# Kernel tuning notes

Hardware: AMD Instinct MI355X
Metric: run time of the kernel (lower is better)

## Reference

```python
import jax, jax.numpy as jnp
import numpy as np

EMBED_DIM = 1024
NUM_HEADS = 16
HEAD_DIM = EMBED_DIM // NUM_HEADS


def setup_inputs() -> dict:
    key = jax.random.key(0)
    ks = jax.random.split(key, 10)
    s = 1.0 / np.sqrt(EMBED_DIM)
    x = jax.random.normal(ks[0], (2, 2048, EMBED_DIM), dtype=jnp.float32)
    Wq = jax.random.uniform(ks[1], (EMBED_DIM, EMBED_DIM), jnp.float32, -s, s)
    bq = jax.random.uniform(ks[2], (EMBED_DIM,), jnp.float32, -s, s)
    Wk = jax.random.uniform(ks[3], (EMBED_DIM, EMBED_DIM), jnp.float32, -s, s)
    bk = jax.random.uniform(ks[4], (EMBED_DIM,), jnp.float32, -s, s)
    Wv = jax.random.uniform(ks[5], (EMBED_DIM, EMBED_DIM), jnp.float32, -s, s)
    bv = jax.random.uniform(ks[6], (EMBED_DIM,), jnp.float32, -s, s)
    Wo = jax.random.uniform(ks[7], (EMBED_DIM, EMBED_DIM), jnp.float32, -s, s)
    bo = jax.random.uniform(ks[8], (EMBED_DIM,), jnp.float32, -s, s)
    return {"x": x, "Wq": Wq, "bq": bq, "Wk": Wk, "bk": bk,
            "Wv": Wv, "bv": bv, "Wo": Wo, "bo": bo}


def reference(x, Wq, bq, Wk, bk, Wv, bv, Wo, bo):
    b, s, e = x.shape
    h, d = NUM_HEADS, HEAD_DIM
    scale = d ** -0.5
    # projections (torch Linear: x @ W.T + b; here W stored as [in, out])
    q = (x @ Wq + bq).reshape(b, s, h, d)
    k = (x @ Wk + bk).reshape(b, s, h, d)
    v = (x @ Wv + bv).reshape(b, s, h, d)
    logits = jnp.einsum('bqhd,bkhd->bhqk', q, k) * scale
    causal = jnp.tril(jnp.ones((s, s), dtype=bool))  # keep lower triangle
    logits = jnp.where(causal, logits, -jnp.inf)
    attn = jax.nn.softmax(logits, axis=-1)
    out = jnp.einsum('bhqk,bkhd->bqhd', attn, v).reshape(b, s, e)
    return out @ Wo + bo
```

## Files before the change

### kernel.cpp

```cpp
#include <hip/hip_runtime.h>


#define EMB 1024
#define SEQ 2048
#define NB 2
#define NH 16
#define HD 64

#define QSCALE 0.18033688011112042f

typedef float f32x4 __attribute__((ext_vector_type(4)));
typedef float f32x16 __attribute__((ext_vector_type(16)));
typedef float floatx4 __attribute__((ext_vector_type(4)));
typedef short short8 __attribute__((ext_vector_type(8)));
typedef __bf16 bf16x8 __attribute__((ext_vector_type(8)));
typedef __bf16 bf16x2 __attribute__((ext_vector_type(2)));
typedef unsigned short ushortx4 __attribute__((ext_vector_type(4)));
typedef unsigned int uintx4 __attribute__((ext_vector_type(4)));
typedef int int2v __attribute__((ext_vector_type(2)));

__device__ __forceinline__ unsigned short bf16u(float f) {
  __bf16 h = (__bf16)f;
  return __builtin_bit_cast(unsigned short, h);
}

__device__ __forceinline__ unsigned pkbf(float lo, float hi) {
  bf16x2 v;
  v[0] = (__bf16)lo;
  v[1] = (__bf16)hi;
  return __builtin_bit_cast(unsigned, v);
}

__device__ __forceinline__ f32x4 mfma16(short8 a, short8 b, f32x4 c) {
  return __builtin_amdgcn_mfma_f32_16x16x32_bf16(
      __builtin_bit_cast(bf16x8, a), __builtin_bit_cast(bf16x8, b), c, 0, 0, 0);
}

__device__ __forceinline__ f32x16 mfma32(short8 a, short8 b, f32x16 c) {
  return __builtin_amdgcn_mfma_f32_32x32x16_bf16(
      __builtin_bit_cast(bf16x8, a), __builtin_bit_cast(bf16x8, b), c, 0, 0, 0);
}

__device__ __forceinline__ void plswap(unsigned& a, unsigned& b) {
  int2v r = __builtin_amdgcn_permlane32_swap((int)a, (int)b, false, false);
  a = (unsigned)r[0];
  b = (unsigned)r[1];
}

__device__ __forceinline__ void gload16(const void* g, void* lds) {
  __builtin_amdgcn_global_load_lds(
      (const __attribute__((address_space(1))) unsigned int*)g,
      (__attribute__((address_space(3))) unsigned int*)lds, 16, 0, 0);
}

__global__ __launch_bounds__(256) void cvt_x_kernel(
    const float* __restrict__ x, unsigned short* __restrict__ out) {
  const int idx = (blockIdx.x * 256 + threadIdx.x) * 4;
  floatx4 v = *(const floatx4*)(x + idx);
  ushortx4 o;
  #pragma unroll
  for (int i = 0; i < 4; ++i) o[i] = bf16u(v[i]);
  *(ushortx4*)(out + idx) = o;
}

__global__ __launch_bounds__(256) void cvt_w4_kernel(
    const float* __restrict__ W0, const float* __restrict__ W1,
    const float* __restrict__ W2, const float* __restrict__ W3,
    unsigned short* __restrict__ T0, unsigned short* __restrict__ T1,
    unsigned short* __restrict__ T2, unsigned short* __restrict__ T3) {
  __shared__ unsigned short tile[32][33];
  const int z = blockIdx.z;
  const float* W = (z == 0) ? W0 : (z == 1) ? W1 : (z == 2) ? W2 : W3;
  unsigned short* WT = (z == 0) ? T0 : (z == 1) ? T1 : (z == 2) ? T2 : T3;
  const int k0 = blockIdx.x * 32, n0 = blockIdx.y * 32;
  const int t = threadIdx.x;
  const int r = t >> 3, c = (t & 7) * 4;
  floatx4 v = *(const floatx4*)(W + (k0 + r) * EMB + n0 + c);
  #pragma unroll
  for (int i = 0; i < 4; ++i) tile[r][c + i] = bf16u(v[i]);
  __syncthreads();
  ushortx4 o;
  #pragma unroll
  for (int i = 0; i < 4; ++i) o[i] = tile[c + i][r];
  *(ushortx4*)(WT + (n0 + r) * EMB + k0 + c) = o;
}

#define GEMM_KLOOP(OP1, OP2)                                                 \
    for (int kk = 0; kk < 64; kk += 32) {                                    \
      short8 a[4], b[4];                                                     \
      _Pragma("unroll")                                                      \
      for (int i = 0; i < 4; ++i)                                            \
        a[i] = *(const short8*)(As + (wr * 64 + i * 16 + ln) * 64 + kk + g * 8); \
      _Pragma("unroll")                                                      \
      for (int j = 0; j < 4; ++j)                                            \
        b[j] = *(const short8*)(Bs + (wc * 64 + j * 16 + ln) * 64 + kk + g * 8); \
      _Pragma("unroll")                                                      \
      for (int i = 0; i < 4; ++i)                                            \
        _Pragma("unroll")                                                    \
        for (int j = 0; j < 4; ++j)                                          \
          acc[i][j] = mfma16(OP1, OP2, acc[i][j]);                           \
    }

#define GEMM_STAGE(Aptr, Bptr, kt_, buf_)                                    \
    do {                                                                     \
      const int kb_ = (kt_) * 64;                                            \
      _Pragma("unroll")                                                      \
      for (int it = 0; it < 4; ++it) {                                       \
        const int chunk = w * 4 + it;                                        \
        const int lin = chunk * 64 + l;                                      \
        const int row = lin >> 3, col = (lin & 7) * 8;                       \
        gload16(Aptr + (m0 + row) * EMB + kb_ + col,                         \
                (char*)&AsB[buf_][0] + chunk * 1024);                        \
        gload16(Bptr + (n0 + row) * EMB + kb_ + col,                         \
                (char*)&BsB[buf_][0] + chunk * 1024);                        \
      }                                                                      \
    } while (0)

__global__ __launch_bounds__(256) void gemm_qkv_kernel(
    const unsigned short* __restrict__ Xb,
    const unsigned short* __restrict__ W0, const unsigned short* __restrict__ W1,
    const unsigned short* __restrict__ W2,
    const float* __restrict__ b0, const float* __restrict__ b1,
    const float* __restrict__ b2,
    unsigned short* __restrict__ Qo, unsigned short* __restrict__ Ko,
    unsigned short* __restrict__ Vo) {
  __shared__ __align__(16) unsigned short AsB[2][128 * 64];
  __shared__ __align__(16) unsigned short BsB[2][128 * 64];
  const int z = blockIdx.z;
  const unsigned short* Wt = (z == 0) ? W0 : ((z == 1) ? W1 : W2);
  const float* bias = (z == 0) ? b0 : ((z == 1) ? b1 : b2);
  const bool sw = (z != 2);
  const int m0 = blockIdx.y * 128, n0 = blockIdx.x * 128;
  const int tid = threadIdx.x, l = tid & 63, w = tid >> 6;
  const int g = l >> 4, ln = l & 15;
  const int wr = w >> 1, wc = w & 1;

  f32x4 acc[4][4];
  #pragma unroll
  for (int i = 0; i < 4; ++i)
    #pragma unroll
    for (int j = 0; j < 4; ++j) acc[i][j] = (f32x4){0.f, 0.f, 0.f, 0.f};

  GEMM_STAGE(Xb, Wt, 0, 0);
  #pragma unroll 1
  for (int kt = 0; kt < 16; ++kt) {
    const int cur = kt & 1;
    if (kt + 1 < 16) {
      GEMM_STAGE(Xb, Wt, kt + 1, cur ^ 1);
      asm volatile("s_waitcnt vmcnt(8)" ::: "memory");
    } else {
      asm volatile("s_waitcnt vmcnt(0)" ::: "memory");
    }
    __builtin_amdgcn_s_barrier();
    const unsigned short* As = &AsB[cur][0];
    const unsigned short* Bs = &BsB[cur][0];
    if (sw) {
      GEMM_KLOOP(b[j], a[i])
    } else {
      GEMM_KLOOP(a[i], b[j])
    }
    asm volatile("" ::: "memory");
    __builtin_amdgcn_s_barrier();
  }

  const int mb = m0 + wr * 64, nb = n0 + wc * 64;
  if (sw) {
    unsigned short* dst = (z == 0) ? Qo : Ko;
    const float osc = (z == 0) ? QSCALE : 1.0f;
    #pragma unroll
    for (int j = 0; j < 4; ++j) {
      const int n = nb + j * 16 + 4 * g;
      floatx4 bv_ = *(const floatx4*)(bias + n);
      const int h = n >> 6, d = n & 63;
      #pragma unroll
      for (int i = 0; i < 4; ++i) {
        const int m = mb + i * 16 + ln;
        const int bb = m >> 11, ss = m & 2047;
        ushortx4 o;
        #pragma unroll
        for (int e = 0; e < 4; ++e) o[e] = bf16u((acc[i][j][e] + bv_[e]) * osc);
        *(ushortx4*)(dst + ((bb * NH + h) * SEQ + ss) * HD + d) = o;
      }
    }
  } else {
    #pragma unroll
    for (int j = 0; j < 4; ++j) {
      const int n = nb + j * 16 + ln;
      const float bgain = bias[n];
      const int h = n >> 6, d = n & 63;
      #pragma unroll
      for (int i = 0; i < 4; ++i) {
        const int mf = mb + i * 16 + 4 * g;
        const int bb = mf >> 11, ss = mf & 2047;
        ushortx4 o;
        #pragma unroll
        for (int e = 0; e < 4; ++e) o[e] = bf16u(acc[i][j][e] + bgain);
        *(ushortx4*)(Vo + ((bb * NH + h) * HD + d) * SEQ + ss) = o;
      }
    }
  }
}

__global__ __launch_bounds__(256) void attn_kernel(
    const unsigned short* __restrict__ Q, const unsigned short* __restrict__ K,
    const unsigned short* __restrict__ Vt, unsigned short* __restrict__ O) {
  __shared__ __align__(16) unsigned short Kt[2][128 * 64];
  __shared__ __align__(16) unsigned short Vl[2][64 * 128];
  const int id = blockIdx.x;
  const int bh = id & 31;
  const int grp = id >> 5;
  const int T = (grp < 8) ? (15 - grp) : (grp - 8);
  const int h = bh & 15, b = bh >> 4;
  const int tid = threadIdx.x, l = tid & 63, w = tid >> 6;
  const int q32 = l & 31;
  const int hi = l >> 5;
  const size_t baseQK = (size_t)bh * SEQ * HD;
  const size_t baseV = (size_t)bh * HD * SEQ;

  const int krw = l >> 3;
  const int kcg = (l & 7) ^ (l >> 3);
  const int vrw = l >> 4;

  const int nkt = T + 1;
  const int qw = T * 128 + w * 32;

  #pragma unroll
  for (int i = 0; i < 4; ++i) {
    const int c = 4 * w + i;
    gload16(K + baseQK + (size_t)(8 * c + krw) * HD + kcg * 8,
            (char*)&Kt[0][0] + c * 1024);
    const int vr = 4 * c + vrw;
    const int vcg = (l & 15) ^ (vr & 15);
    gload16(Vt + baseV + (size_t)vr * SEQ + vcg * 8,
            (char*)&Vl[0][0] + c * 1024);
  }

  const int qrow = qw + q32;
  short8 qf[4];
  #pragma unroll
  for (int ds = 0; ds < 4; ++ds)
    qf[ds] = *(const short8*)(Q + baseQK + (size_t)qrow * HD + ds * 16 + hi * 8);

  float m_run = -1e30f, l_run = 0.f;
  f32x16 acc[2];
  #pragma unroll
  for (int dh = 0; dh < 2; ++dh)
    #pragma unroll
    for (int r = 0; r < 16; ++r) acc[dh][r] = 0.f;

  #pragma unroll 1
  for (int kt = 0; kt < nkt; ++kt) {
    const int cur = kt & 1;
    const bool has_next = (kt + 1 < nkt);
    if (has_next) {
      const int nxt = cur ^ 1;
      const size_t kof = (size_t)(kt + 1) * 128;
      #pragma unroll
      for (int i = 0; i < 4; ++i) {
        const int c = 4 * w + i;
        gload16(K + baseQK + (kof + 8 * c + krw) * HD + kcg * 8,
                (char*)&Kt[nxt][0] + c * 1024);
        const int vr = 4 * c + vrw;
        const int vcg = (l & 15) ^ (vr & 15);
        gload16(Vt + baseV + (size_t)vr * SEQ + kof + vcg * 8,
                (char*)&Vl[nxt][0] + c * 1024);
      }
      asm volatile("s_waitcnt vmcnt(8)" ::: "memory");
    } else {
      asm volatile("s_waitcnt vmcnt(0)" ::: "memory");
    }
    __builtin_amdgcn_s_barrier();

    const bool last = (kt == T);

    f32x16 sv[4];
    #pragma unroll
    for (int kj = 0; kj < 4; ++kj)
      #pragma unroll
      for (int r = 0; r < 16; ++r) sv[kj][r] = -1e30f;

    __builtin_amdgcn_s_setprio(1);
    #pragma unroll
    for (int kj = 0; kj < 4; ++kj) {
      if (!last || kj <= w) {
        f32x16 t;
        #pragma unroll
        for (int r = 0; r < 16; ++r) t[r] = 0.f;
        #pragma unroll
        for (int ds = 0; ds < 4; ++ds) {
          short8 kf = *(const short8*)(
              &Kt[cur][(kj * 32 + q32) * 64 + (((ds * 2 + hi) ^ (l & 7)) * 8)]);
          t = mfma32(kf, qf[ds], t);
        }
        if (last && kj == w) {
          #pragma unroll
          for (int r = 0; r < 16; ++r) {
            const int crow = (r & 3) + 8 * (r >> 2) + 4 * hi;
            sv[kj][r] = (crow <= q32) ? t[r] : -1e30f;
          }
        } else {
          sv[kj] = t;
        }
      }
    }
    __builtin_amdgcn_s_setprio(0);

    float tm = -1e30f;
    #pragma unroll
    for (int kj = 0; kj < 4; ++kj)
      #pragma unroll
      for (int r = 0; r < 16; ++r) tm = fmaxf(tm, sv[kj][r]);
    tm = fmaxf(tm, __shfl_xor(tm, 32));
    const float nm = fmaxf(m_run, tm);
    const float al = exp2f(m_run - nm);
    m_run = nm;

    #pragma unroll
    for (int r = 0; r < 16; ++r) {
      const int crb = (r & 3) + 8 * (r >> 2);
      const float ar = __shfl(al, crb + 4 * hi);
      acc[0][r] *= ar;
      acc[1][r] *= ar;
    }

    float rs = 0.f;
    short8 pa[8];
    #pragma unroll
    for (int kj = 0; kj < 4; ++kj) {
      if (!last || kj <= w) {
        float p[16];
        #pragma unroll
        for (int r = 0; r < 16; ++r) {
          p[r] = exp2f(sv[kj][r] - nm);
          rs += p[r];
        }
        unsigned A0 = pkbf(p[0], p[1]);
        unsigned B0 = pkbf(p[2], p[3]);
        unsigned C0 = pkbf(p[4], p[5]);
        unsigned D0 = pkbf(p[6], p[7]);
        plswap(A0, C0);
        plswap(B0, D0);
        uintx4 u0;
        u0[0] = A0; u0[1] = B0; u0[2] = C0; u0[3] = D0;
        pa[2 * kj] = __builtin_bit_cast(short8, u0);
        unsigned A1 = pkbf(p[8], p[9]);
        unsigned B1 = pkbf(p[10], p[11]);
        unsigned C1 = pkbf(p[12], p[13]);
        unsigned D1 = pkbf(p[14], p[15]);
        plswap(A1, C1);
        plswap(B1, D1);
        uintx4 u1;
        u1[0] = A1; u1[1] = B1; u1[2] = C1; u1[3] = D1;
        pa[2 * kj + 1] = __builtin_bit_cast(short8, u1);
      }
    }
    rs += __shfl_xor(rs, 32);
    l_run = l_run * al + rs;

    const int smax = last ? (2 * w + 2) : 8;
    __builtin_amdgcn_s_setprio(1);
    #pragma unroll
    for (int dh = 0; dh < 2; ++dh) {
      #pragma unroll
      for (int s = 0; s < 8; ++s) {
        if (s < smax) {
          short8 vb = *(const short8*)(
              &Vl[cur][(32 * dh + q32) * 128 + (((s * 2 + hi) ^ (l & 15)) * 8)]);
          acc[dh] = mfma32(pa[s], vb, acc[dh]);
        }
      }
    }
    __builtin_amdgcn_s_setprio(0);

    asm volatile("" ::: "memory");
    __builtin_amdgcn_s_barrier();
  }

  const float inv = 1.f / l_run;
  #pragma unroll
  for (int dh = 0; dh < 2; ++dh) {
    #pragma unroll
    for (int r = 0; r < 16; ++r) {
      const int crb = (r & 3) + 8 * (r >> 2);
      const float ir = __shfl(inv, crb + 4 * hi);
      const int q = qw + crb + 4 * hi;
      O[((size_t)b * SEQ + q) * EMB + h * HD + 32 * dh + q32] =
          bf16u(acc[dh][r] * ir);
    }
  }
}

__global__ __launch_bounds__(256) void gemm_o_kernel(
    const unsigned short* __restrict__ Ab, const unsigned short* __restrict__ Wt,
    const float* __restrict__ bias, float* __restrict__ out) {
  __shared__ __align__(16) unsigned short AsB[2][128 * 64];
  __shared__ __align__(16) unsigned short BsB[2][128 * 64];
  const int m0 = blockIdx.y * 128, n0 = blockIdx.x * 128;
  const int tid = threadIdx.x, l = tid & 63, w = tid >> 6;
  const int g = l >> 4, ln = l & 15;
  const int wr = w >> 1, wc = w & 1;

  f32x4 acc[4][4];
  #pragma unroll
  for (int i = 0; i < 4; ++i)
    #pragma unroll
    for (int j = 0; j < 4; ++j) acc[i][j] = (f32x4){0.f, 0.f, 0.f, 0.f};

  GEMM_STAGE(Ab, Wt, 0, 0);
  #pragma unroll 1
  for (int kt = 0; kt < 16; ++kt) {
    const int cur = kt & 1;
    if (kt + 1 < 16) {
      GEMM_STAGE(Ab, Wt, kt + 1, cur ^ 1);
      asm volatile("s_waitcnt vmcnt(8)" ::: "memory");
    } else {
      asm volatile("s_waitcnt vmcnt(0)" ::: "memory");
    }
    __builtin_amdgcn_s_barrier();
    const unsigned short* As = &AsB[cur][0];
    const unsigned short* Bs = &BsB[cur][0];
    GEMM_KLOOP(b[j], a[i])
    asm volatile("" ::: "memory");
    __builtin_amdgcn_s_barrier();
  }

  const int mb = m0 + wr * 64, nb = n0 + wc * 64;
  #pragma unroll
  for (int j = 0; j < 4; ++j) {
    const int n = nb + j * 16 + 4 * g;
    floatx4 bv_ = *(const floatx4*)(bias + n);
    #pragma unroll
    for (int i = 0; i < 4; ++i) {
      const int m = mb + i * 16 + ln;
      floatx4 o = acc[i][j] + bv_;
      *(floatx4*)(out + (size_t)m * EMB + n) = o;
    }
  }
}

extern "C" void kernel_launch(void* const* d_in, const int* in_sizes, int n_in,
                              void* d_out, int out_size, void* d_ws, size_t ws_size,
                              hipStream_t stream) {
  const float* x  = (const float*)d_in[0];
  const float* Wq = (const float*)d_in[1];
  const float* bq = (const float*)d_in[2];
  const float* Wk = (const float*)d_in[3];
  const float* bk = (const float*)d_in[4];
  const float* Wv = (const float*)d_in[5];
  const float* bv = (const float*)d_in[6];
  const float* Wo = (const float*)d_in[7];
  const float* bo = (const float*)d_in[8];
  float* out = (float*)d_out;

  char* ws = (char*)d_ws;
  unsigned short* Xb  = (unsigned short*)(ws);
  unsigned short* WqT = (unsigned short*)(ws + 8388608);
  unsigned short* WkT = (unsigned short*)(ws + 10485760);
  unsigned short* WvT = (unsigned short*)(ws + 12582912);
  unsigned short* WoT = (unsigned short*)(ws + 14680064);
  unsigned short* Qb  = (unsigned short*)(ws + 16777216);
  unsigned short* Kb  = (unsigned short*)(ws + 25165824);
  unsigned short* Vtb = (unsigned short*)(ws + 33554432);
  unsigned short* Ao  = Xb;

  hipLaunchKernelGGL(cvt_x_kernel, dim3(4096), dim3(256), 0, stream, x, Xb);
  hipLaunchKernelGGL(cvt_w4_kernel, dim3(32, 32, 4), dim3(256), 0, stream,
                     Wq, Wk, Wv, Wo, WqT, WkT, WvT, WoT);
  hipLaunchKernelGGL(gemm_qkv_kernel, dim3(8, 32, 3), dim3(256), 0, stream,
                     Xb, WqT, WkT, WvT, bq, bk, bv, Qb, Kb, Vtb);
  hipLaunchKernelGGL(attn_kernel, dim3(512), dim3(256), 0, stream,
                     Qb, Kb, Vtb, Ao);
  hipLaunchKernelGGL(gemm_o_kernel, dim3(8, 32), dim3(256), 0, stream,
                     Ao, WoT, bo, out);
}
```

Before: 173.4 us.

## Shrink attention tiles to 64 queries and 64 keys with two-wave blocks

Retiles the causal attention kernel: each block now handles 64 query rows with 2 waves (128 threads) and streams 64-key K/V tiles, giving 1024 blocks instead of 512. The LDS swizzle is reworked for 64-wide rows and the diagonal masking logic is adjusted. The aim is better load balance and occupancy across the GPU's CUs and less wasted work on diagonal tiles. In exchange, each K/V tile is reused by fewer query rows, so global K/V traffic roughly doubles, and there are more loop iterations with their barrier overhead.

Result: no change. 170.2 us (-1.8%).

```diff
diff --git a/kernel.cpp b/kernel.cpp
--- a/kernel.cpp
+++ b/kernel.cpp
@@ -201,15 +201,15 @@
   }
 }
 
-__global__ __launch_bounds__(256) void attn_kernel(
+__global__ __launch_bounds__(128) void attn_kernel(
     const unsigned short* __restrict__ Q, const unsigned short* __restrict__ K,
     const unsigned short* __restrict__ Vt, unsigned short* __restrict__ O) {
-  __shared__ __align__(16) unsigned short Kt[2][128 * 64];
-  __shared__ __align__(16) unsigned short Vl[2][64 * 128];
+  __shared__ __align__(16) unsigned short Kt[2][64 * 64];
+  __shared__ __align__(16) unsigned short Vl[2][64 * 64];
   const int id = blockIdx.x;
   const int bh = id & 31;
   const int grp = id >> 5;
-  const int T = (grp < 8) ? (15 - grp) : (grp - 8);
+  const int qt = (grp < 16) ? (31 - grp) : (grp - 16);
   const int h = bh & 15, b = bh >> 4;
   const int tid = threadIdx.x, l = tid & 63, w = tid >> 6;
   const int q32 = l & 31;
@@ -217,22 +217,19 @@
   const size_t baseQK = (size_t)bh * SEQ * HD;
   const size_t baseV = (size_t)bh * HD * SEQ;
 
-  const int krw = l >> 3;
-  const int kcg = (l & 7) ^ (l >> 3);
-  const int vrw = l >> 4;
-
-  const int nkt = T + 1;
-  const int qw = T * 128 + w * 32;
+  const int rw8 = l >> 3;
+  const int cg8 = l & 7;
+
+  const int nkt = qt + 1;
+  const int qw = qt * 64 + 32 * w;
 
   #pragma unroll
   for (int i = 0; i < 4; ++i) {
     const int c = 4 * w + i;
-    gload16(K + baseQK + (size_t)(8 * c + krw) * HD + kcg * 8,
-            (char*)&Kt[0][0] + c * 1024);
-    const int vr = 4 * c + vrw;
-    const int vcg = (l & 15) ^ (vr & 15);
-    gload16(Vt + baseV + (size_t)vr * SEQ + vcg * 8,
-            (char*)&Vl[0][0] + c * 1024);
+    const int kr = 8 * c + rw8;
+    const int kg = cg8 ^ (kr & 7);
+    gload16(K + baseQK + (size_t)kr * HD + kg * 8, (char*)&Kt[0][0] + c * 1024);
+    gload16(Vt + baseV + (size_t)kr * SEQ + kg * 8, (char*)&Vl[0][0] + c * 1024);
   }
 
   const int qrow = qw + q32;
@@ -254,15 +251,15 @@
     const bool has_next = (kt + 1 < nkt);
     if (has_next) {
       const int nxt = cur ^ 1;
-      const size_t kof = (size_t)(kt + 1) * 128;
+      const size_t kof = (size_t)(kt + 1) * 64;
       #pragma unroll
       for (int i = 0; i < 4; ++i) {
         const int c = 4 * w + i;
-        gload16(K + baseQK + (kof + 8 * c + krw) * HD + kcg * 8,
+        const int kr = 8 * c + rw8;
+        const int kg = cg8 ^ (kr & 7);
+        gload16(K + baseQK + (kof + kr) * HD + kg * 8,
                 (char*)&Kt[nxt][0] + c * 1024);
-        const int vr = 4 * c + vrw;
-        const int vcg = (l & 15) ^ (vr & 15);
-        gload16(Vt + baseV + (size_t)vr * SEQ + kof + vcg * 8,
+        gload16(Vt + baseV + (size_t)kr * SEQ + kof + kg * 8,
                 (char*)&Vl[nxt][0] + c * 1024);
       }
       asm volatile("s_waitcnt vmcnt(8)" ::: "memory");
@@ -271,25 +268,26 @@
     }
     __builtin_amdgcn_s_barrier();
 
-    const bool last = (kt == T);
-
-    f32x16 sv[4];
-    #pragma unroll
-    for (int kj = 0; kj < 4; ++kj)
+    const bool last = (kt == qt);
+    const int jmax = last ? w : 1;
+
+    f32x16 sv[2];
+    #pragma unroll
+    for (int kj = 0; kj < 2; ++kj)
       #pragma unroll
       for (int r = 0; r < 16; ++r) sv[kj][r] = -1e30f;
 
     __builtin_amdgcn_s_setprio(1);
     #pragma unroll
-    for (int kj = 0; kj < 4; ++kj) {
-      if (!last || kj <= w) {
+    for (int kj = 0; kj < 2; ++kj) {
+      if (kj <= jmax) {
         f32x16 t;
         #pragma unroll
         for (int r = 0; r < 16; ++r) t[r] = 0.f;
         #pragma unroll
         for (int ds = 0; ds < 4; ++ds) {
           short8 kf = *(const short8*)(
-              &Kt[cur][(kj * 32 + q32) * 64 + (((ds * 2 + hi) ^ (l & 7)) * 8)]);
+              &Kt[cur][(kj * 32 + q32) * 64 + (((ds * 2 + hi) ^ (q32 & 7)) * 8)]);
           t = mfma32(kf, qf[ds], t);
         }
         if (last && kj == w) {
@@ -307,7 +305,7 @@
 
     float tm = -1e30f;
     #pragma unroll
-    for (int kj = 0; kj < 4; ++kj)
+    for (int kj = 0; kj < 2; ++kj)
       #pragma unroll
       for (int r = 0; r < 16; ++r) tm = fmaxf(tm, sv[kj][r]);
     tm = fmaxf(tm, __shfl_xor(tm, 32));
@@ -324,10 +322,10 @@
     }
 
     float rs = 0.f;
-    short8 pa[8];
-    #pragma unroll
-    for (int kj = 0; kj < 4; ++kj) {
-      if (!last || kj <= w) {
+    short8 pa[4];
+    #pragma unroll
+    for (int kj = 0; kj < 2; ++kj) {
+      if (kj <= jmax) {
         float p[16];
         #pragma unroll
         for (int r = 0; r < 16; ++r) {
@@ -357,15 +355,15 @@
     rs += __shfl_xor(rs, 32);
     l_run = l_run * al + rs;
 
-    const int smax = last ? (2 * w + 2) : 8;
+    const int smax = last ? (2 * w + 2) : 4;
     __builtin_amdgcn_s_setprio(1);
     #pragma unroll
     for (int dh = 0; dh < 2; ++dh) {
       #pragma unroll
-      for (int s = 0; s < 8; ++s) {
+      for (int s = 0; s < 4; ++s) {
         if (s < smax) {
           short8 vb = *(const short8*)(
-              &Vl[cur][(32 * dh + q32) * 128 + (((s * 2 + hi) ^ (l & 15)) * 8)]);
+              &Vl[cur][(32 * dh + q32) * 64 + (((s * 2 + hi) ^ (q32 & 7)) * 8)]);
           acc[dh] = mfma32(pa[s], vb, acc[dh]);
         }
       }
@@ -468,7 +466,7 @@
                      Wq, Wk, Wv, Wo, WqT, WkT, WvT, WoT);
   hipLaunchKernelGGL(gemm_qkv_kernel, dim3(8, 32, 3), dim3(256), 0, stream,
                      Xb, WqT, WkT, WvT, bq, bk, bv, Qb, Kb, Vtb);
-  hipLaunchKernelGGL(attn_kernel, dim3(512), dim3(256), 0, stream,
+  hipLaunchKernelGGL(attn_kernel, dim3(1024), dim3(128), 0, stream,
                      Qb, Kb, Vtb, Ao);
   hipLaunchKernelGGL(gemm_o_kernel, dim3(8, 32), dim3(256), 0, stream,
                      Ao, WoT, bo, out);
```

## Split attention KV range across two blocks and merge with combine kernel

Applied to the files above, without the earlier changes.

The attention kernel now splits each query tile's causal KV range into two halves handled by separate blocks (1024 blocks instead of 512). Each half writes unnormalized bf16 partial outputs plus per-row max and sum, and a new combine kernel merges them. This balances work across CUs and shortens the longest block's critical path. It costs an extra launch, extra global traffic for the partials, and one more bf16 rounding. The x and weight conversion kernels are also merged into a single launch.

Result: faster. 163.3 us (-5.8%).

```diff
diff --git a/kernel.cpp b/kernel.cpp
--- a/kernel.cpp
+++ b/kernel.cpp
@@ -24,6 +24,10 @@
   return __builtin_bit_cast(unsigned short, h);
 }
 
+__device__ __forceinline__ float bf2f(unsigned short u) {
+  return __builtin_bit_cast(float, ((unsigned)u) << 16);
+}
+
 __device__ __forceinline__ unsigned pkbf(float lo, float hi) {
   bf16x2 v;
   v[0] = (__bf16)lo;
@@ -53,27 +57,32 @@
       (__attribute__((address_space(3))) unsigned int*)lds, 16, 0, 0);
 }
 
-__global__ __launch_bounds__(256) void cvt_x_kernel(
-    const float* __restrict__ x, unsigned short* __restrict__ out) {
-  const int idx = (blockIdx.x * 256 + threadIdx.x) * 4;
-  floatx4 v = *(const floatx4*)(x + idx);
-  ushortx4 o;
-  #pragma unroll
-  for (int i = 0; i < 4; ++i) o[i] = bf16u(v[i]);
-  *(ushortx4*)(out + idx) = o;
-}
-
-__global__ __launch_bounds__(256) void cvt_w4_kernel(
+__global__ __launch_bounds__(256) void cvt_all_kernel(
+    const float* __restrict__ x, unsigned short* __restrict__ Xb,
     const float* __restrict__ W0, const float* __restrict__ W1,
     const float* __restrict__ W2, const float* __restrict__ W3,
     unsigned short* __restrict__ T0, unsigned short* __restrict__ T1,
     unsigned short* __restrict__ T2, unsigned short* __restrict__ T3) {
+  const int z = blockIdx.z;
+  const int t = threadIdx.x;
+  if (z == 4) {
+    const int blin = blockIdx.y * 32 + blockIdx.x;
+    const int base = blin * 4096 + t * 4;
+    #pragma unroll
+    for (int c = 0; c < 4; ++c) {
+      const int idx = base + c * 1024;
+      floatx4 v = *(const floatx4*)(x + idx);
+      ushortx4 o;
+      #pragma unroll
+      for (int i = 0; i < 4; ++i) o[i] = bf16u(v[i]);
+      *(ushortx4*)(Xb + idx) = o;
+    }
+    return;
+  }
   __shared__ unsigned short tile[32][33];
-  const int z = blockIdx.z;
   const float* W = (z == 0) ? W0 : (z == 1) ? W1 : (z == 2) ? W2 : W3;
   unsigned short* WT = (z == 0) ? T0 : (z == 1) ? T1 : (z == 2) ? T2 : T3;
   const int k0 = blockIdx.x * 32, n0 = blockIdx.y * 32;
-  const int t = threadIdx.x;
   const int r = t >> 3, c = (t & 7) * 4;
   floatx4 v = *(const floatx4*)(W + (k0 + r) * EMB + n0 + c);
   #pragma unroll
@@ -203,14 +212,21 @@
 
 __global__ __launch_bounds__(256) void attn_kernel(
     const unsigned short* __restrict__ Q, const unsigned short* __restrict__ K,
-    const unsigned short* __restrict__ Vt, unsigned short* __restrict__ O) {
+    const unsigned short* __restrict__ Vt,
+    unsigned short* __restrict__ Opart, float* __restrict__ mlbuf) {
   __shared__ __align__(16) unsigned short Kt[2][128 * 64];
   __shared__ __align__(16) unsigned short Vl[2][64 * 128];
   const int id = blockIdx.x;
-  const int bh = id & 31;
-  const int grp = id >> 5;
-  const int T = (grp < 8) ? (15 - grp) : (grp - 8);
-  const int h = bh & 15, b = bh >> 4;
+  const int j = id >> 8;
+  const int slot = id & 255;
+  const int bh = slot & 31;
+  const int p = slot >> 5;
+  const int T = (j < 2) ? (15 - p) : p;
+  const int half = j & 1;
+  const int na = (T + 2) >> 1;
+  const int kt0 = half ? na : 0;
+  const int kt1 = half ? (T + 1) : na;
+  const int len = kt1 - kt0;
   const int tid = threadIdx.x, l = tid & 63, w = tid >> 6;
   const int q32 = l & 31;
   const int hi = l >> 5;
@@ -221,25 +237,7 @@
   const int kcg = (l & 7) ^ (l >> 3);
   const int vrw = l >> 4;
 
-  const int nkt = T + 1;
   const int qw = T * 128 + w * 32;
-
-  #pragma unroll
-  for (int i = 0; i < 4; ++i) {
-    const int c = 4 * w + i;
-    gload16(K + baseQK + (size_t)(8 * c + krw) * HD + kcg * 8,
-            (char*)&Kt[0][0] + c * 1024);
-    const int vr = 4 * c + vrw;
-    const int vcg = (l & 15) ^ (vr & 15);
-    gload16(Vt + baseV + (size_t)vr * SEQ + vcg * 8,
-            (char*)&Vl[0][0] + c * 1024);
-  }
-
-  const int qrow = qw + q32;
-  short8 qf[4];
-  #pragma unroll
-  for (int ds = 0; ds < 4; ++ds)
-    qf[ds] = *(const short8*)(Q + baseQK + (size_t)qrow * HD + ds * 16 + hi * 8);
 
   float m_run = -1e30f, l_run = 0.f;
   f32x16 acc[2];
@@ -248,145 +246,202 @@
     #pragma unroll
     for (int r = 0; r < 16; ++r) acc[dh][r] = 0.f;
 
-  #pragma unroll 1
-  for (int kt = 0; kt < nkt; ++kt) {
-    const int cur = kt & 1;
-    const bool has_next = (kt + 1 < nkt);
-    if (has_next) {
-      const int nxt = cur ^ 1;
-      const size_t kof = (size_t)(kt + 1) * 128;
+  if (len > 0) {
+    {
+      const size_t kof = (size_t)kt0 * 128;
       #pragma unroll
       for (int i = 0; i < 4; ++i) {
         const int c = 4 * w + i;
         gload16(K + baseQK + (kof + 8 * c + krw) * HD + kcg * 8,
-                (char*)&Kt[nxt][0] + c * 1024);
+                (char*)&Kt[0][0] + c * 1024);
         const int vr = 4 * c + vrw;
         const int vcg = (l & 15) ^ (vr & 15);
         gload16(Vt + baseV + (size_t)vr * SEQ + kof + vcg * 8,
-                (char*)&Vl[nxt][0] + c * 1024);
-      }
-      asm volatile("s_waitcnt vmcnt(8)" ::: "memory");
-    } else {
-      asm volatile("s_waitcnt vmcnt(0)" ::: "memory");
-    }
-    __builtin_amdgcn_s_barrier();
-
-    const bool last = (kt == T);
-
-    f32x16 sv[4];
-    #pragma unroll
-    for (int kj = 0; kj < 4; ++kj)
-      #pragma unroll
-      for (int r = 0; r < 16; ++r) sv[kj][r] = -1e30f;
-
-    __builtin_amdgcn_s_setprio(1);
-    #pragma unroll
-    for (int kj = 0; kj < 4; ++kj) {
-      if (!last || kj <= w) {
-        f32x16 t;
+                (char*)&Vl[0][0] + c * 1024);
+      }
+    }
+
+    const int qrow = qw + q32;
+    short8 qf[4];
+    #pragma unroll
+    for (int ds = 0; ds < 4; ++ds)
+      qf[ds] = *(const short8*)(Q + baseQK + (size_t)qrow * HD + ds * 16 + hi * 8);
+
+    #pragma unroll 1
+    for (int kt = kt0; kt < kt1; ++kt) {
+      const int cur = (kt - kt0) & 1;
+      const bool has_next = (kt + 1 < kt1);
+      if (has_next) {
+        const int nxt = cur ^ 1;
+        const size_t kof = (size_t)(kt + 1) * 128;
         #pragma unroll
-        for (int r = 0; r < 16; ++r) t[r] = 0.f;
+        for (int i = 0; i < 4; ++i) {
+          const int c = 4 * w + i;
+          gload16(K + baseQK + (kof + 8 * c + krw) * HD + kcg * 8,
+                  (char*)&Kt[nxt][0] + c * 1024);
+          const int vr = 4 * c + vrw;
+          const int vcg = (l & 15) ^ (vr & 15);
+          gload16(Vt + baseV + (size_t)vr * SEQ + kof + vcg * 8,
+                  (char*)&Vl[nxt][0] + c * 1024);
+        }
+        asm volatile("s_waitcnt vmcnt(8)" ::: "memory");
+      } else {
+        asm volatile("s_waitcnt vmcnt(0)" ::: "memory");
+      }
+      __builtin_amdgcn_s_barrier();
+
+      const bool last = (kt == T);
+
+      f32x16 sv[4];
+      #pragma unroll
+      for (int kj = 0; kj < 4; ++kj)
         #pragma unroll
-        for (int ds = 0; ds < 4; ++ds) {
-          short8 kf = *(const short8*)(
-              &Kt[cur][(kj * 32 + q32) * 64 + (((ds * 2 + hi) ^ (l & 7)) * 8)]);
-          t = mfma32(kf, qf[ds], t);
+        for (int r = 0; r < 16; ++r) sv[kj][r] = -1e30f;
+
+      __builtin_amdgcn_s_setprio(1);
+      #pragma unroll
+      for (int kj = 0; kj < 4; ++kj) {
+        if (!last || kj <= w) {
+          f32x16 t;
+          #pragma unroll
+          for (int r = 0; r < 16; ++r) t[r] = 0.f;
+          #pragma unroll
+          for (int ds = 0; ds < 4; ++ds) {
+            short8 kf = *(const short8*)(
+                &Kt[cur][(kj * 32 + q32) * 64 + (((ds * 2 + hi) ^ (l & 7)) * 8)]);
+            t = mfma32(kf, qf[ds], t);
+          }
+          if (last && kj == w) {
+            #pragma unroll
+            for (int r = 0; r < 16; ++r) {
+              const int crow = (r & 3) + 8 * (r >> 2) + 4 * hi;
+              sv[kj][r] = (crow <= q32) ? t[r] : -1e30f;
+            }
+          } else {
+            sv[kj] = t;
+          }
         }
-        if (last && kj == w) {
+      }
+      __builtin_amdgcn_s_setprio(0);
+
+      float tm = -1e30f;
+      #pragma unroll
+      for (int kj = 0; kj < 4; ++kj)
+        #pragma unroll
+        for (int r = 0; r < 16; ++r) tm = fmaxf(tm, sv[kj][r]);
+      tm = fmaxf(tm, __shfl_xor(tm, 32));
+      const float nm = fmaxf(m_run, tm);
+      const float al = exp2f(m_run - nm);
+      m_run = nm;
+
+      #pragma unroll
+      for (int r = 0; r < 16; ++r) {
+        const int crb = (r & 3) + 8 * (r >> 2);
+        const float ar = __shfl(al, crb + 4 * hi);
+        acc[0][r] *= ar;
+        acc[1][r] *= ar;
+      }
+
+      float rs = 0.f;
+      short8 pa[8];
+      #pragma unroll
+      for (int kj = 0; kj < 4; ++kj) {
+        if (!last || kj <= w) {
+          float pv[16];
           #pragma unroll
           for (int r = 0; r < 16; ++r) {
-            const int crow = (r & 3) + 8 * (r >> 2) + 4 * hi;
-            sv[kj][r] = (crow <= q32) ? t[r] : -1e30f;
+            pv[r] = exp2f(sv[kj][r] - nm);
+            rs += pv[r];
           }
-        } else {
-          sv[kj] = t;
+          unsigned A0 = pkbf(pv[0], pv[1]);
+          unsigned B0 = pkbf(pv[2], pv[3]);
+          unsigned C0 = pkbf(pv[4], pv[5]);
+          unsigned D0 = pkbf(pv[6], pv[7]);
+          plswap(A0, C0);
+          plswap(B0, D0);
+          uintx4 u0;
+          u0[0] = A0; u0[1] = B0; u0[2] = C0; u0[3] = D0;
+          pa[2 * kj] = __builtin_bit_cast(short8, u0);
+          unsigned A1 = pkbf(pv[8], pv[9]);
+          unsigned B1 = pkbf(pv[10], pv[11]);
+          unsigned C1 = pkbf(pv[12], pv[13]);
+          unsigned D1 = pkbf(pv[14], pv[15]);
+          plswap(A1, C1);
+          plswap(B1, D1);
+          uintx4 u1;
+          u1[0] = A1; u1[1] = B1; u1[2] = C1; u1[3] = D1;
+          pa[2 * kj + 1] = __builtin_bit_cast(short8, u1);
         }
       }
-    }
-    __builtin_amdgcn_s_setprio(0);
-
-    float tm = -1e30f;
-    #pragma unroll
-    for (int kj = 0; kj < 4; ++kj)
-      #pragma unroll
-      for (int r = 0; r < 16; ++r) tm = fmaxf(tm, sv[kj][r]);
-    tm = fmaxf(tm, __shfl_xor(tm, 32));
-    const float nm = fmaxf(m_run, tm);
-    const float al = exp2f(m_run - nm);
-    m_run = nm;
-
+      rs += __shfl_xor(rs, 32);
+      l_run = l_run * al + rs;
+
+      const int smax = last ? (2 * w + 2) : 8;
+      __builtin_amdgcn_s_setprio(1);
+      #pragma unroll
+      for (int dh = 0; dh < 2; ++dh) {
+        #pragma unroll
+        for (int s = 0; s < 8; ++s) {
+          if (s < smax) {
+            short8 vb = *(const short8*)(
+                &Vl[cur][(32 * dh + q32) * 128 + (((s * 2 + hi) ^ (l & 15)) * 8)]);
+            acc[dh] = mfma32(pa[s], vb, acc[dh]);
+          }
+        }
+      }
+      __builtin_amdgcn_s_setprio(0);
+
+      asm volatile("" ::: "memory");
+      __builtin_amdgcn_s_barrier();
+    }
+  }
+
+  const int blk = bh * 16 + T;
+  const int pbase = ((blk * 2 + half) * 128) * 64;
+  #pragma unroll
+  for (int dh = 0; dh < 2; ++dh) {
     #pragma unroll
     for (int r = 0; r < 16; ++r) {
-      const int crb = (r & 3) + 8 * (r >> 2);
-      const float ar = __shfl(al, crb + 4 * hi);
-      acc[0][r] *= ar;
-      acc[1][r] *= ar;
-    }
-
-    float rs = 0.f;
-    short8 pa[8];
-    #pragma unroll
-    for (int kj = 0; kj < 4; ++kj) {
-      if (!last || kj <= w) {
-        float p[16];
-        #pragma unroll
-        for (int r = 0; r < 16; ++r) {
-          p[r] = exp2f(sv[kj][r] - nm);
-          rs += p[r];
-        }
-        unsigned A0 = pkbf(p[0], p[1]);
-        unsigned B0 = pkbf(p[2], p[3]);
-        unsigned C0 = pkbf(p[4], p[5]);
-        unsigned D0 = pkbf(p[6], p[7]);
-        plswap(A0, C0);
-        plswap(B0, D0);
-        uintx4 u0;
-        u0[0] = A0; u0[1] = B0; u0[2] = C0; u0[3] = D0;
-        pa[2 * kj] = __builtin_bit_cast(short8, u0);
-        unsigned A1 = pkbf(p[8], p[9]);
-        unsigned B1 = pkbf(p[10], p[11]);
-        unsigned C1 = pkbf(p[12], p[13]);
-        unsigned D1 = pkbf(p[14], p[15]);
-        plswap(A1, C1);
-        plswap(B1, D1);
-        uintx4 u1;
-        u1[0] = A1; u1[1] = B1; u1[2] = C1; u1[3] = D1;
-        pa[2 * kj + 1] = __builtin_bit_cast(short8, u1);
-      }
-    }
-    rs += __shfl_xor(rs, 32);
-    l_run = l_run * al + rs;
-
-    const int smax = last ? (2 * w + 2) : 8;
-    __builtin_amdgcn_s_setprio(1);
-    #pragma unroll
-    for (int dh = 0; dh < 2; ++dh) {
-      #pragma unroll
-      for (int s = 0; s < 8; ++s) {
-        if (s < smax) {
-          short8 vb = *(const short8*)(
-              &Vl[cur][(32 * dh + q32) * 128 + (((s * 2 + hi) ^ (l & 15)) * 8)]);
-          acc[dh] = mfma32(pa[s], vb, acc[dh]);
-        }
-      }
-    }
-    __builtin_amdgcn_s_setprio(0);
-
-    asm volatile("" ::: "memory");
-    __builtin_amdgcn_s_barrier();
-  }
-
-  const float inv = 1.f / l_run;
-  #pragma unroll
-  for (int dh = 0; dh < 2; ++dh) {
-    #pragma unroll
-    for (int r = 0; r < 16; ++r) {
-      const int crb = (r & 3) + 8 * (r >> 2);
-      const float ir = __shfl(inv, crb + 4 * hi);
-      const int q = qw + crb + 4 * hi;
-      O[((size_t)b * SEQ + q) * EMB + h * HD + 32 * dh + q32] =
-          bf16u(acc[dh][r] * ir);
-    }
+      const int ql = w * 32 + (r & 3) + 8 * (r >> 2) + 4 * hi;
+      Opart[pbase + ql * 64 + 32 * dh + q32] = bf16u(acc[dh][r]);
+    }
+  }
+  if (l < 32) {
+    const int mb = blk * 512 + half * 256;
+    mlbuf[mb + w * 32 + q32] = m_run;
+    mlbuf[mb + 128 + w * 32 + q32] = l_run;
+  }
+}
+
+__global__ __launch_bounds__(256) void combine_kernel(
+    const unsigned short* __restrict__ Opart, const float* __restrict__ mlbuf,
+    unsigned short* __restrict__ Ao) {
+  const int blk = blockIdx.x;
+  const int bh = blk >> 4, T = blk & 15;
+  const int h = bh & 15, b = bh >> 4;
+  const int t = threadIdx.x;
+  const int d0 = (t & 15) * 4;
+  const int p0 = (blk * 2 + 0) * 128 * 64;
+  const int p1 = (blk * 2 + 1) * 128 * 64;
+  #pragma unroll 1
+  for (int pass = 0; pass < 8; ++pass) {
+    const int ql = pass * 16 + (t >> 4);
+    const float m0 = mlbuf[blk * 512 + ql];
+    const float l0 = mlbuf[blk * 512 + 128 + ql];
+    const float m1 = mlbuf[blk * 512 + 256 + ql];
+    const float l1 = mlbuf[blk * 512 + 384 + ql];
+    const float m = fmaxf(m0, m1);
+    const float w0 = exp2f(m0 - m);
+    const float w1 = exp2f(m1 - m);
+    const float inv = 1.f / (w0 * l0 + w1 * l1);
+    ushortx4 a0 = *(const ushortx4*)(Opart + p0 + ql * 64 + d0);
+    ushortx4 a1 = *(const ushortx4*)(Opart + p1 + ql * 64 + d0);
+    ushortx4 o;
+    #pragma unroll
+    for (int e = 0; e < 4; ++e)
+      o[e] = bf16u((w0 * bf2f(a0[e]) + w1 * bf2f(a1[e])) * inv);
+    const int q = T * 128 + ql;
+    *(ushortx4*)(Ao + ((size_t)(b * SEQ + q)) * EMB + h * HD + d0) = o;
   }
 }
 
@@ -462,14 +517,17 @@
   unsigned short* Kb  = (unsigned short*)(ws + 25165824);
   unsigned short* Vtb = (unsigned short*)(ws + 33554432);
   unsigned short* Ao  = Xb;
-
-  hipLaunchKernelGGL(cvt_x_kernel, dim3(4096), dim3(256), 0, stream, x, Xb);
-  hipLaunchKernelGGL(cvt_w4_kernel, dim3(32, 32, 4), dim3(256), 0, stream,
-                     Wq, Wk, Wv, Wo, WqT, WkT, WvT, WoT);
+  unsigned short* Opart = (unsigned short*)d_out;
+  float* mlbuf = (float*)WqT;
+
+  hipLaunchKernelGGL(cvt_all_kernel, dim3(32, 32, 5), dim3(256), 0, stream,
+                     x, Xb, Wq, Wk, Wv, Wo, WqT, WkT, WvT, WoT);
   hipLaunchKernelGGL(gemm_qkv_kernel, dim3(8, 32, 3), dim3(256), 0, stream,
                      Xb, WqT, WkT, WvT, bq, bk, bv, Qb, Kb, Vtb);
-  hipLaunchKernelGGL(attn_kernel, dim3(512), dim3(256), 0, stream,
-                     Qb, Kb, Vtb, Ao);
+  hipLaunchKernelGGL(attn_kernel, dim3(1024), dim3(256), 0, stream,
+                     Qb, Kb, Vtb, Opart, mlbuf);
+  hipLaunchKernelGGL(combine_kernel, dim3(512), dim3(256), 0, stream,
+                     Opart, mlbuf, Ao);
   hipLaunchKernelGGL(gemm_o_kernel, dim3(8, 32), dim3(256), 0, stream,
                      Ao, WoT, bo, out);
 }
```
